# Kernel tuning notes

Hardware: AMD Instinct MI355X
Metric: run time of the kernel (lower is better)

## Reference

```python
import jax, jax.numpy as jnp
import numpy as np

TEMP = 0.05
BG_KNN = 50
POSK = 3
BAL_W = 0.15
P = 32768   # num proxies in memory bank
D = 256     # feature dim
C = 8       # num cameras (proxy p has camera p % C, pseudo-label p // C)
N = 65536   # dataset size
B = 256     # batch


def setup_inputs() -> dict:
    key = jax.random.key(0)
    k1, k2, k3, k4 = jax.random.split(key, 4)
    mem = jax.random.normal(k1, (P, D), jnp.float32)
    mem = mem / jnp.linalg.norm(mem, axis=1, keepdims=True)  # L2-normalized bank
    features = jax.random.normal(k2, (B, D), jnp.float32)
    all_proxy_label = jax.random.randint(k3, (N,), 0, P, jnp.int32)
    all_pseudo_label = all_proxy_label // C          # consistent with label_proxies layout
    targets = jax.random.randint(k4, (B,), 0, N, jnp.int32)
    cams = all_proxy_label[targets] % C              # each sample's camera owns its target proxy
    Pc = P // C
    cam_proxies = (jnp.arange(C)[:, None] + C * jnp.arange(Pc)[None, :]).astype(jnp.int32)   # [C, Pc]
    label_proxies = (jnp.arange(P // C)[:, None] * C + jnp.arange(C)[None, :]).astype(jnp.int32)  # [num_ids, C]
    return dict(features=features, targets=targets, cams=cams, epoch=0,
                global_memory=mem, all_pseudo_label=all_pseudo_label,
                all_proxy_label=all_proxy_label, cam_proxies=cam_proxies,
                label_proxies=label_proxies)


def _cam_mean_sum(per_sample, cams, num_cams):
    # original: for each camera, mean loss over that camera's samples, then sum over cameras
    s = jax.ops.segment_sum(per_sample, cams, num_segments=num_cams)
    n = jax.ops.segment_sum(jnp.ones_like(per_sample), cams, num_segments=num_cams)
    return jnp.where(n > 0, s / jnp.maximum(n, 1.0), 0.0).sum()


def _forward(features, global_memory, targets, cams, all_pseudo_label,
             all_proxy_label, cam_proxies, label_proxies):
    pseudo_y = all_pseudo_label[targets]      # [B]
    prx = all_proxy_label[targets]            # [B]
    num_cams = cam_proxies.shape[0]
    Bsz = features.shape[0]
    rows = jnp.arange(Bsz)

    # ExemplarMemory: score = features @ memory^T; backward treats memory as constant
    score = features @ jax.lax.stop_gradient(global_memory).T   # [B, P]
    inputs = score / TEMP

    # --- intra-camera loss: log-softmax over this sample's camera proxies ---
    cam_prx = cam_proxies[cams]                                   # [B, Pc]
    sel = jnp.take_along_axis(inputs, cam_prx, axis=1)            # [B, Pc]
    mask = (cam_prx == prx[:, None]).astype(inputs.dtype)
    intra = -(jax.nn.log_softmax(sel, axis=1) * mask).sum(axis=1)

    # --- cross-camera proxy-associate loss: positives + bg_knn hardest negatives ---
    pos = label_proxies[pseudo_y]                                 # [B, K]
    K = pos.shape[1]
    temp = jax.lax.stop_gradient(inputs).at[rows[:, None], pos].set(10000.0)
    _, top_idx = jax.lax.top_k(temp, BG_KNN + K)                  # descending: positives first
    sel2 = jnp.take_along_axis(inputs, top_idx, axis=1)           # [B, bg_knn+K]
    tgt2 = jnp.concatenate([jnp.full((K,), 1.0 / K, inputs.dtype),
                            jnp.zeros((BG_KNN,), inputs.dtype)])
    cross = -(jax.nn.log_softmax(sel2, axis=1) * tgt2).sum(axis=1)

    # --- online camera-wise NN-enhance loss ---
    mem = jax.lax.stop_gradient(global_memory)
    sims = BAL_W * jax.lax.stop_gradient(score) + (1.0 - BAL_W) * (mem[prx] @ mem.T)  # [B, P]
    sims_by_cam = sims[:, cam_proxies]                            # [B, C, Pc]
    arg = jnp.argmax(sims_by_cam, axis=2)                         # [B, C] best proxy per camera
    tops = cam_proxies[jnp.arange(num_cams)[None, :], arg]        # [B, C]
    top_vals = jnp.take_along_axis(sims, tops, axis=1)            # [B, C]
    _, sel_c = jax.lax.top_k(top_vals, POSK)                      # posK strongest camera-tops
    chosen = jnp.take_along_axis(tops, sel_c, axis=1)             # [B, posK]
    sims = sims.at[rows[:, None], chosen].set(10000.0)
    _, top3 = jax.lax.top_k(sims, BG_KNN + POSK)                  # positives first (descending)
    sel3 = jnp.take_along_axis(inputs, top3, axis=1)
    tgt3 = jnp.concatenate([jnp.full((POSK,), 1.0 / POSK, inputs.dtype),
                            jnp.zeros((BG_KNN,), inputs.dtype)])
    online = -(jax.nn.log_softmax(sel3, axis=1) * tgt3).sum(axis=1)

    return (_cam_mean_sum(intra, cams, num_cams)
            + _cam_mean_sum(cross, cams, num_cams)
            + _cam_mean_sum(online, cams, num_cams))


def reference(features, targets, cams, epoch, global_memory, all_pseudo_label,
              all_proxy_label, cam_proxies, label_proxies):
    return _forward(features, global_memory, targets, cams,
                    all_pseudo_label, all_proxy_label, cam_proxies, label_proxies)
```

## Files before the change

kernel.cpp:

```cpp
#include <hip/hip_runtime.h>

#define P_CNT 32768
#define D_DIM 256
#define B_SZ  256
#define NTHR  1024
#define NW    16
#define INVT  20.0f
#define NEG_BIG -3.0e38f

typedef _Float16 half8  __attribute__((ext_vector_type(8)));
typedef _Float16 half4v __attribute__((ext_vector_type(4)));
typedef float    floatx4 __attribute__((ext_vector_type(4)));

__device__ __forceinline__ float blockMax(float v, int tid, float* redW) {
#pragma unroll
  for (int off = 1; off < 64; off <<= 1) v = fmaxf(v, __shfl_xor(v, off));
  if ((tid & 63) == 0) redW[tid >> 6] = v;
  __syncthreads();
  float r = redW[0];
#pragma unroll
  for (int w = 1; w < NW; ++w) r = fmaxf(r, redW[w]);
  __syncthreads();
  return r;
}

__device__ __forceinline__ float blockSum(float v, int tid, float* redW) {
#pragma unroll
  for (int off = 1; off < 64; off <<= 1) v += __shfl_xor(v, off);
  if ((tid & 63) == 0) redW[tid >> 6] = v;
  __syncthreads();
  float r = 0.f;
#pragma unroll
  for (int w = 0; w < NW; ++w) r += redW[w];
  __syncthreads();
  return r;
}

template <typename GetV>
__device__ __forceinline__ float radixSelectReg(GetV getv, int k, int tid,
                                                int* histW , int* histT ,
                                                float* bufV , int* cntS,
                                                float* bcast) {
  const int lane = tid & 63, wid = tid >> 6;
  unsigned prefix = 0;
  int krem = k;
  int shift = 28;
  for (;;) {
    unsigned long long accLo = 0ull, accHi = 0ull;
    const int sh4 = shift + 4;
#pragma unroll
    for (int j = 0; j < 32; ++j) {
      float v = getv(j);
      unsigned bu = __float_as_uint(v);
      unsigned key = bu ^ ((unsigned)(((int)bu) >> 31) | 0x80000000u);
      bool ok = (sh4 >= 32) || ((key >> sh4) == prefix);
      int bin = (key >> shift) & 15;
      unsigned long long one = ok ? 1ull : 0ull;
      if (bin < 8) accLo += one << (bin << 3);
      else         accHi += one << ((bin - 8) << 3);
    }
    int cnt[16];
#pragma unroll
    for (int j = 0; j < 8; ++j) cnt[j] = (int)((accLo >> (j * 8)) & 0xffull);
#pragma unroll
    for (int j = 0; j < 8; ++j) cnt[8 + j] = (int)((accHi >> (j * 8)) & 0xffull);
#pragma unroll
    for (int j = 0; j < 16; ++j) {
      int v = cnt[j];
#pragma unroll
      for (int off = 1; off < 64; off <<= 1) v += __shfl_xor(v, off);
      cnt[j] = v;
    }
    if (lane == 0) {
#pragma unroll
      for (int j = 0; j < 16; ++j) histW[wid * 16 + j] = cnt[j];
    }
    __syncthreads();
    if (tid < 16) {
      int sacc = 0;
#pragma unroll
      for (int w = 0; w < NW; ++w) sacc += histW[w * 16 + tid];
      histT[tid] = sacc;
    }
    __syncthreads();
    int t = -1, above = 0, cntT = 0;
#pragma unroll
    for (int j = 15; j >= 0; --j) {
      int tj = histT[j];
      if (t < 0) {
        if (above + tj >= krem) { t = j; cntT = tj; }
        else above += tj;
      }
    }
    krem -= above;
    prefix = (prefix << 4) | (unsigned)t;
    if (cntT <= 64 || shift == 0) break;
    shift -= 4;
  }
  if (tid == 0) cntS[0] = 0;
  __syncthreads();
#pragma unroll
  for (int j = 0; j < 32; ++j) {
    float v = getv(j);
    unsigned bu = __float_as_uint(v);
    unsigned key = bu ^ ((unsigned)(((int)bu) >> 31) | 0x80000000u);
    if ((key >> shift) == prefix) {
      int p = atomicAdd(cntS, 1);
      if (p < 64) bufV[p] = v;
    }
  }
  __syncthreads();
  if (tid < 64) {
    int n = min(cntS[0], 64);
    float vl = (tid < n) ? bufV[tid] : NEG_BIG;
    float vkv = NEG_BIG;
    for (int it = 0; it < krem; ++it) {
      float wv = vl;
#pragma unroll
      for (int off = 1; off < 64; off <<= 1) wv = fmaxf(wv, __shfl_xor(wv, off));
      if (it == krem - 1) vkv = wv;
      unsigned long long m = __ballot(vl == wv);
      int fl = (int)__ffsll(m) - 1;
      if (tid == fl) vl = NEG_BIG;
    }
    if (tid == 0) bcast[0] = vkv;
  }
  __syncthreads();
  float r = bcast[0];
  __syncthreads();
  return r;
}

__global__ void prep_kernel(const float* __restrict__ features,
                            const int* __restrict__ targets,
                            const int* __restrict__ all_prx,
                            const float* __restrict__ mem,
                            float* __restrict__ A2,
                            int* __restrict__ prxArr) {
  const int b = blockIdx.x;
  const int k = threadIdx.x;
  const int t = targets[b];
  const int pr = all_prx[t];
  if (k == 0) prxArr[b] = pr;
  A2[b * D_DIM + k] = features[b * D_DIM + k];
  A2[(B_SZ + b) * D_DIM + k] = mem[(size_t)pr * D_DIM + k];
}

__global__ __launch_bounds__(256) void gemm_mfma(const float* __restrict__ A,
                                                 const float* __restrict__ Bm,
                                                 float* __restrict__ Co) {
  __shared__ _Float16 Ah[128][32], Al[128][32], Bh[128][32], Bl[128][32];
  const int tid = threadIdx.x;
  const int lane = tid & 63;
  const int wid = tid >> 6;
  const int wr = wid >> 1, wc = wid & 1;
  const int orig = (blockIdx.x & 7) * 128 + (blockIdx.x >> 3);
  const int rowBase = (orig & 3) << 7;
  const int colBase = (orig >> 2) << 7;

  const int trow = tid >> 3;
  const int tseg = tid & 7;

  floatx4 acc[4][4];
#pragma unroll
  for (int i = 0; i < 4; ++i)
#pragma unroll
    for (int j = 0; j < 4; ++j) {
      acc[i][j][0] = 0.f; acc[i][j][1] = 0.f; acc[i][j][2] = 0.f; acc[i][j][3] = 0.f;
    }

  const int fr = lane & 15;
  const int kg = (lane >> 4) << 3;

  for (int step = 0; step < 8; ++step) {
    const int k0 = step << 5;
    float4 sa[4], sb[4];
#pragma unroll
    for (int p = 0; p < 4; ++p) {
      const int r = trow + (p << 5);
      sa[p] = *(const float4*)(A  + (size_t)(rowBase + r) * D_DIM + k0 + tseg * 4);
      sb[p] = *(const float4*)(Bm + (size_t)(colBase + r) * D_DIM + k0 + tseg * 4);
    }
    __syncthreads();
#pragma unroll
    for (int p = 0; p < 4; ++p) {
      const int r = trow + (p << 5);
      float4 v = sa[p];
      half4v h, l;
      h[0] = (_Float16)v.x; l[0] = (_Float16)(v.x - (float)h[0]);
      h[1] = (_Float16)v.y; l[1] = (_Float16)(v.y - (float)h[1]);
      h[2] = (_Float16)v.z; l[2] = (_Float16)(v.z - (float)h[2]);
      h[3] = (_Float16)v.w; l[3] = (_Float16)(v.w - (float)h[3]);
      *(half4v*)&Ah[r][tseg * 4] = h;
      *(half4v*)&Al[r][tseg * 4] = l;
      v = sb[p];
      h[0] = (_Float16)v.x; l[0] = (_Float16)(v.x - (float)h[0]);
      h[1] = (_Float16)v.y; l[1] = (_Float16)(v.y - (float)h[1]);
      h[2] = (_Float16)v.z; l[2] = (_Float16)(v.z - (float)h[2]);
      h[3] = (_Float16)v.w; l[3] = (_Float16)(v.w - (float)h[3]);
      *(half4v*)&Bh[r][tseg * 4] = h;
      *(half4v*)&Bl[r][tseg * 4] = l;
    }
    __syncthreads();
    half8 ah[4], al[4], bh[4], bl[4];
#pragma unroll
    for (int f = 0; f < 4; ++f) {
      ah[f] = *(const half8*)&Ah[wr * 64 + f * 16 + fr][kg];
      al[f] = *(const half8*)&Al[wr * 64 + f * 16 + fr][kg];
      bh[f] = *(const half8*)&Bh[wc * 64 + f * 16 + fr][kg];
      bl[f] = *(const half8*)&Bl[wc * 64 + f * 16 + fr][kg];
    }
#pragma unroll
    for (int fm = 0; fm < 4; ++fm)
#pragma unroll
      for (int fn = 0; fn < 4; ++fn) {
        acc[fm][fn] = __builtin_amdgcn_mfma_f32_16x16x32_f16(ah[fm], bh[fn], acc[fm][fn], 0, 0, 0);
        acc[fm][fn] = __builtin_amdgcn_mfma_f32_16x16x32_f16(ah[fm], bl[fn], acc[fm][fn], 0, 0, 0);
        acc[fm][fn] = __builtin_amdgcn_mfma_f32_16x16x32_f16(al[fm], bh[fn], acc[fm][fn], 0, 0, 0);
      }
  }
  const int rsub = (lane >> 4) << 2;
#pragma unroll
  for (int fm = 0; fm < 4; ++fm)
#pragma unroll
    for (int fn = 0; fn < 4; ++fn) {
      const int r0 = rowBase + wr * 64 + fm * 16 + rsub;
      const int c0 = colBase + wc * 64 + fn * 16 + fr;
#pragma unroll
      for (int r = 0; r < 4; ++r)
        Co[(size_t)(r0 + r) * P_CNT + c0] = acc[fm][fn][r];
    }
}

__global__ __launch_bounds__(NTHR) void persample(const float* __restrict__ OUT,
                                                  const int* __restrict__ cams,
                                                  const int* __restrict__ prxArr,
                                                  float* __restrict__ intraArr,
                                                  float* __restrict__ crossArr,
                                                  float* __restrict__ onlArr) {
  __shared__ int   histW[NW * 16];
  __shared__ int   histT[16];
  __shared__ float bufV[64];
  __shared__ int   bufI[32];
  __shared__ int   cntS[4];
  __shared__ float redW[NW];
  __shared__ float sv[64];
  __shared__ int   si[64];
  __shared__ float cvW[NW * 8];
  __shared__ int   ciW[NW * 8];
  __shared__ float mw[NW], sw[NW];
  __shared__ float bcast[2];

  const int b = blockIdx.x;
  const int tid = threadIdx.x;
  const int lane = tid & 63, wid = tid >> 6;
  const float* Srow = OUT + (size_t)b * P_CNT;
  const float* Mrow = OUT + (size_t)(B_SZ + b) * P_CNT;
  const int pr = prxArr[b];
  const int cam = cams[b];
  const int base4 = tid << 2;

  float s[32];
#pragma unroll
  for (int q = 0; q < 8; ++q) {
    float4 f = ((const float4*)Srow)[tid + (q << 10)];
    s[4 * q + 0] = f.x; s[4 * q + 1] = f.y; s[4 * q + 2] = f.z; s[4 * q + 3] = f.w;
  }
  float pmax = NEG_BIG;
#pragma unroll
  for (int j = 0; j < 32; ++j) pmax = fmaxf(pmax, s[j]);
  const float M = blockMax(pmax, tid, redW);

  {
    const bool mine = ((tid & 1) == (cam >> 2));
    const int cc = cam & 3;
    float im = NEG_BIG, is = 0.f;
    if (mine) {
#pragma unroll
      for (int q = 0; q < 8; ++q) {
        float v = (cc == 0) ? s[4 * q] : (cc == 1) ? s[4 * q + 1]
                : (cc == 2) ? s[4 * q + 2] : s[4 * q + 3];
        if (v <= im) is += expf((v - im) * INVT);
        else { is = is * expf((im - v) * INVT) + 1.f; im = v; }
      }
    }
#pragma unroll
    for (int off = 1; off < 64; off <<= 1) {
      float m2 = __shfl_xor(im, off);
      float s2 = __shfl_xor(is, off);
      float Mx = fmaxf(im, m2);
      is = is * expf((im - Mx) * INVT) + s2 * expf((m2 - Mx) * INVT);
      im = Mx;
    }
    if (lane == 0) { mw[wid] = im; sw[wid] = is; }
  }
  __syncthreads();
  if (tid == 0) {
    float m0 = mw[0], s0 = sw[0];
    for (int w = 1; w < NW; ++w) {
      float Mx = fmaxf(m0, mw[w]);
      s0 = s0 * expf((m0 - Mx) * INVT) + sw[w] * expf((mw[w] - Mx) * INVT);
      m0 = Mx;
    }
    intraArr[b] = -((Srow[pr] - m0) * INVT - logf(s0));
  }

  const int posBase = pr & ~7;
  if (tid < 8) sv[tid] = Srow[posBase + tid];
  __syncthreads();
  auto crossVal = [&](int j) -> float {
    int p = base4 + ((j >> 2) << 12) + (j & 3);
    return ((unsigned)(p - posBase) < 8u) ? NEG_BIG : s[j];
  };
  const float vk = radixSelectReg(crossVal, 50, tid, histW, histT, bufV, cntS, bcast);
  {
    float se = 0.f, cg = 0.f;
#pragma unroll
    for (int j = 0; j < 32; ++j) {
      float v = crossVal(j);
      if (v > vk) { se += expf((v - M) * INVT); cg += 1.f; }
    }
    se = blockSum(se, tid, redW);
    cg = blockSum(cg, tid, redW);
    if (tid == 0) {
      float stot = se + (50.f - cg) * expf((vk - M) * INVT);
      for (int p = 0; p < 8; ++p) stot += expf((sv[p] - M) * INVT);
      float lse = logf(stot);
      float acc = 0.f;
      for (int p = 0; p < 8; ++p) acc += (sv[p] - M) * INVT - lse;
      crossArr[b] = -acc * 0.125f;
    }
  }

#pragma unroll
  for (int q = 0; q < 8; ++q) {
    float4 m2 = ((const float4*)Mrow)[tid + (q << 10)];
    s[4 * q + 0] = 0.15f * s[4 * q + 0] + 0.85f * m2.x;
    s[4 * q + 1] = 0.15f * s[4 * q + 1] + 0.85f * m2.y;
    s[4 * q + 2] = 0.15f * s[4 * q + 2] + 0.85f * m2.z;
    s[4 * q + 3] = 0.15f * s[4 * q + 3] + 0.85f * m2.w;
  }

  {
    float cm[4] = {NEG_BIG, NEG_BIG, NEG_BIG, NEG_BIG};
    int cix[4] = {0x7fffffff, 0x7fffffff, 0x7fffffff, 0x7fffffff};
#pragma unroll
    for (int q = 0; q < 8; ++q) {
#pragma unroll
      for (int c = 0; c < 4; ++c) {
        float v = s[4 * q + c];
        int p = base4 + (q << 12) + c;
        if (v > cm[c]) { cm[c] = v; cix[c] = p; }
      }
    }
    const bool odd = (tid & 1);
    float v8[8]; int i8[8];
#pragma unroll
    for (int c = 0; c < 4; ++c) {
      float ov = __shfl_xor(cm[c], 1); int oi = __shfl_xor(cix[c], 1);
      v8[c]     = odd ? ov : cm[c];   i8[c]     = odd ? oi : cix[c];
      v8[c + 4] = odd ? cm[c] : ov;   i8[c + 4] = odd ? cix[c] : oi;
    }
#pragma unroll
    for (int off = 2; off <= 32; off <<= 1) {
#pragma unroll
      for (int c = 0; c < 8; ++c) {
        float vv = __shfl_xor(v8[c], off);
        int   ii = __shfl_xor(i8[c], off);
        if (vv > v8[c] || (vv == v8[c] && ii < i8[c])) { v8[c] = vv; i8[c] = ii; }
      }
    }
    if (lane < 8) {
#pragma unroll
      for (int c = 0; c < 8; ++c)
        if (lane == c) { cvW[wid * 8 + c] = v8[c]; ciW[wid * 8 + c] = i8[c]; }
    }
    __syncthreads();
    if (tid < 8) {
      float v = cvW[tid]; int ix = ciW[tid];
      for (int w = 1; w < NW; ++w) {
        float v2 = cvW[w * 8 + tid]; int i2 = ciW[w * 8 + tid];
        if (v2 > v || (v2 == v && i2 < ix)) { v = v2; ix = i2; }
      }
      cvW[tid] = v; ciW[tid] = ix;
    }
    __syncthreads();
    if (tid == 0) {
      unsigned used = 0;
      for (int k = 0; k < 3; ++k) {
        float best = NEG_BIG; int bc = 0;
        for (int c = 0; c < 8; ++c)
          if (!((used >> c) & 1u) && cvW[c] > best) { best = cvW[c]; bc = c; }
        used |= 1u << bc;
        si[k] = ciW[bc];
      }
    }
    __syncthreads();
  }
  const int c0 = si[0], c1 = si[1], c2 = si[2];
  __syncthreads();

  auto simsVal = [&](int j) -> float {
    int p = base4 + ((j >> 2) << 12) + (j & 3);
    return (p == c0 || p == c1 || p == c2) ? NEG_BIG : s[j];
  };
  const float vk2 = radixSelectReg(simsVal, 50, tid, histW, histT, bufV, cntS, bcast);
  if (tid == 0) { cntS[1] = 0; cntS[2] = 0; }
  __syncthreads();
#pragma unroll
  for (int j = 0; j < 32; ++j) {
    float v = simsVal(j);
    int p = base4 + ((j >> 2) << 12) + (j & 3);
    if (v > vk2) {
      int t = atomicAdd(&cntS[1], 1);
      if (t < 50) si[3 + t] = p;
    } else if (v == vk2) {
      int t = atomicAdd(&cntS[2], 1);
      if (t < 32) bufI[t] = p;
    }
  }
  __syncthreads();
  {
    const int cg = cntS[1];
    const int fill = 50 - cg;
    if (tid < 64) {
      int ne = min(cntS[2], 32);
      int il = (tid < ne) ? bufI[tid] : 0x7fffffff;
      for (int it = 0; it < fill; ++it) {
        int wi = il;
#pragma unroll
        for (int off = 1; off < 64; off <<= 1) wi = min(wi, __shfl_xor(wi, off));
        if (tid == 0) si[3 + cg + it] = wi;
        if (il == wi) il = 0x7fffffff;
      }
    }
  }
  __syncthreads();
  if (tid < 53) sv[tid] = Srow[si[tid]];
  __syncthreads();
  if (tid < 64) {
    float v = (tid < 53) ? sv[tid] : NEG_BIG;
    float mm = v;
#pragma unroll
    for (int off = 1; off < 64; off <<= 1) mm = fmaxf(mm, __shfl_xor(mm, off));
    float e = (tid < 53) ? expf((v - mm) * INVT) : 0.f;
    float ss = e;
#pragma unroll
    for (int off = 1; off < 64; off <<= 1) ss += __shfl_xor(ss, off);
    float lse = logf(ss);
    float c = (tid < 3) ? ((v - mm) * INVT - lse) : 0.f;
#pragma unroll
    for (int off = 1; off < 64; off <<= 1) c += __shfl_xor(c, off);
    if (tid == 0) onlArr[b] = -c * (1.0f / 3.0f);
  }
}

__global__ void finalize(const int* __restrict__ cams,
                         const float* __restrict__ ia,
                         const float* __restrict__ ca,
                         const float* __restrict__ oa,
                         float* __restrict__ out) {
  if (blockIdx.x == 0 && threadIdx.x == 0) {
    float s[8] = {}; float n[8] = {};
    for (int b = 0; b < B_SZ; ++b) {
      int c = cams[b];
      s[c] += ia[b] + ca[b] + oa[b];
      n[c] += 1.f;
    }
    float tot = 0.f;
    for (int c = 0; c < 8; ++c)
      if (n[c] > 0.f) tot += s[c] / n[c];
    out[0] = tot;
  }
}

extern "C" void kernel_launch(void* const* d_in, const int* in_sizes, int n_in,
                              void* d_out, int out_size, void* d_ws, size_t ws_size,
                              hipStream_t stream) {
  const float* features = (const float*)d_in[0];
  const int*   targets  = (const int*)d_in[1];
  const int*   cams     = (const int*)d_in[2];
  const float* mem      = (const float*)d_in[4];
  const int*   all_prx  = (const int*)d_in[6];

  float* ws = (float*)d_ws;
  float* A2  = ws;
  float* OUT = ws + 512 * D_DIM;
  float* tail = OUT + (size_t)512 * P_CNT;
  int*   prxArr  = (int*)tail;
  float* intraArr = (float*)(prxArr + B_SZ);
  float* crossArr = intraArr + B_SZ;
  float* onlArr   = crossArr + B_SZ;

  prep_kernel<<<B_SZ, D_DIM, 0, stream>>>(features, targets, all_prx, mem, A2, prxArr);
  gemm_mfma<<<1024, 256, 0, stream>>>(A2, mem, OUT);
  persample<<<B_SZ, NTHR, 0, stream>>>(OUT, cams, prxArr, intraArr, crossArr, onlArr);
  finalize<<<1, 64, 0, stream>>>(cams, intraArr, crossArr, onlArr, (float*)d_out);
}
```

Measured before the change: 178.4 us.

## Replace 4-bit radix select with 13-bit shared-memory histogram select

The top-k threshold search switches from a 16-bin, 4-bits-per-pass radix select using packed register counters and wave shuffles to an 8192-bin histogram built with LDS atomics, consuming 13 bits per pass. Each pass clears the histogram, bins the matching keys, then uses a block-wide suffix scan to find the bin that holds the k-th largest value. The aim is to cut the number of passes and barriers from up to eight to about two or three. In exchange it adds a 32KB shared histogram, which may lower occupancy, plus atomic contention and clearing cost on every pass.

```diff
diff --git a/kernel.cpp b/kernel.cpp
--- a/kernel.cpp
+++ b/kernel.cpp
@@ -37,65 +37,68 @@
 }
 
 template <typename GetV>
-__device__ __forceinline__ float radixSelectReg(GetV getv, int k, int tid,
-                                                int* histW , int* histT ,
-                                                float* bufV , int* cntS,
-                                                float* bcast) {
+__device__ __forceinline__ float histSelectK(GetV getv, int k, int tid,
+                                             int* hist , int* wt ,
+                                             int* ibc , float* bufV ,
+                                             int* cntS, float* bcast) {
   const int lane = tid & 63, wid = tid >> 6;
+  int shift = 19, prevShift = 32;
   unsigned prefix = 0;
   int krem = k;
-  int shift = 28;
   for (;;) {
-    unsigned long long accLo = 0ull, accHi = 0ull;
-    const int sh4 = shift + 4;
+    {
+      int4* h4 = (int4*)hist;
+      h4[tid] = make_int4(0, 0, 0, 0);
+      h4[tid + 1024] = make_int4(0, 0, 0, 0);
+    }
+    __syncthreads();
 #pragma unroll
     for (int j = 0; j < 32; ++j) {
       float v = getv(j);
       unsigned bu = __float_as_uint(v);
       unsigned key = bu ^ ((unsigned)(((int)bu) >> 31) | 0x80000000u);
-      bool ok = (sh4 >= 32) || ((key >> sh4) == prefix);
-      int bin = (key >> shift) & 15;
-      unsigned long long one = ok ? 1ull : 0ull;
-      if (bin < 8) accLo += one << (bin << 3);
-      else         accHi += one << ((bin - 8) << 3);
-    }
-    int cnt[16];
-#pragma unroll
-    for (int j = 0; j < 8; ++j) cnt[j] = (int)((accLo >> (j * 8)) & 0xffull);
-#pragma unroll
-    for (int j = 0; j < 8; ++j) cnt[8 + j] = (int)((accHi >> (j * 8)) & 0xffull);
-#pragma unroll
-    for (int j = 0; j < 16; ++j) {
-      int v = cnt[j];
-#pragma unroll
-      for (int off = 1; off < 64; off <<= 1) v += __shfl_xor(v, off);
-      cnt[j] = v;
-    }
-    if (lane == 0) {
-#pragma unroll
-      for (int j = 0; j < 16; ++j) histW[wid * 16 + j] = cnt[j];
-    }
-    __syncthreads();
-    if (tid < 16) {
-      int sacc = 0;
-#pragma unroll
-      for (int w = 0; w < NW; ++w) sacc += histW[w * 16 + tid];
-      histT[tid] = sacc;
-    }
-    __syncthreads();
-    int t = -1, above = 0, cntT = 0;
-#pragma unroll
-    for (int j = 15; j >= 0; --j) {
-      int tj = histT[j];
-      if (t < 0) {
-        if (above + tj >= krem) { t = j; cntT = tj; }
-        else above += tj;
-      }
-    }
-    krem -= above;
-    prefix = (prefix << 4) | (unsigned)t;
+      bool ok = (prevShift >= 32) || ((key >> prevShift) == prefix);
+      if (ok) atomicAdd(&hist[(key >> shift) & 8191], 1);
+    }
+    __syncthreads();
+    int bcnt[8];
+    int L = 0;
+#pragma unroll
+    for (int j = 0; j < 8; ++j) { bcnt[j] = hist[8 * tid + j]; L += bcnt[j]; }
+    int S = L;
+#pragma unroll
+    for (int off = 1; off < 64; off <<= 1) {
+      int y = __shfl_down(S, off);
+      S += (lane + off < 64) ? y : 0;
+    }
+    if (lane == 0) wt[wid] = S;
+    __syncthreads();
+    int aboveW = 0;
+    for (int w = wid + 1; w < NW; ++w) aboveW += wt[w];
+    const int R = S + aboveW;
+    const int aboveR = R - L;
+    if (aboveR < krem && krem <= R) {
+      int above = aboveR;
+      int bsel = -1, csel = 0;
+#pragma unroll
+      for (int j = 7; j >= 0; --j) {
+        if (bsel < 0) {
+          if (above + bcnt[j] >= krem) { bsel = 8 * tid + j; csel = bcnt[j]; }
+          else above += bcnt[j];
+        }
+      }
+      ibc[0] = bsel; ibc[1] = krem - above; ibc[2] = csel;
+    }
+    __syncthreads();
+    const int bstar = ibc[0];
+    krem = ibc[1];
+    const int cntT = ibc[2];
+    __syncthreads();
+    const int gap = prevShift - shift;
+    prefix = (prefix << gap) | ((unsigned)bstar & ((1u << gap) - 1u));
+    prevShift = shift;
     if (cntT <= 64 || shift == 0) break;
-    shift -= 4;
+    shift = (shift >= 13) ? (shift - 13) : 0;
   }
   if (tid == 0) cntS[0] = 0;
   __syncthreads();
@@ -104,7 +107,7 @@
     float v = getv(j);
     unsigned bu = __float_as_uint(v);
     unsigned key = bu ^ ((unsigned)(((int)bu) >> 31) | 0x80000000u);
-    if ((key >> shift) == prefix) {
+    if ((key >> prevShift) == prefix) {
       int p = atomicAdd(cntS, 1);
       if (p < 64) bufV[p] = v;
     }
@@ -238,8 +241,9 @@
                                                   float* __restrict__ intraArr,
                                                   float* __restrict__ crossArr,
                                                   float* __restrict__ onlArr) {
-  __shared__ int   histW[NW * 16];
-  __shared__ int   histT[16];
+  __shared__ int   hist[8192];
+  __shared__ int   wt[NW];
+  __shared__ int   ibc[4];
   __shared__ float bufV[64];
   __shared__ int   bufI[32];
   __shared__ int   cntS[4];
@@ -312,7 +316,7 @@
     int p = base4 + ((j >> 2) << 12) + (j & 3);
     return ((unsigned)(p - posBase) < 8u) ? NEG_BIG : s[j];
   };
-  const float vk = radixSelectReg(crossVal, 50, tid, histW, histT, bufV, cntS, bcast);
+  const float vk = histSelectK(crossVal, 50, tid, hist, wt, ibc, bufV, cntS, bcast);
   {
     float se = 0.f, cg = 0.f;
 #pragma unroll
@@ -404,7 +408,7 @@
     int p = base4 + ((j >> 2) << 12) + (j & 3);
     return (p == c0 || p == c1 || p == c2) ? NEG_BIG : s[j];
   };
-  const float vk2 = radixSelectReg(simsVal, 50, tid, histW, histT, bufV, cntS, bcast);
+  const float vk2 = histSelectK(simsVal, 50, tid, hist, wt, ibc, bufV, cntS, bcast);
   if (tid == 0) { cntS[1] = 0; cntS[2] = 0; }
   __syncthreads();
 #pragma unroll
```

After: 143.7 us. 1.24x faster.
